# Performance work log

Hardware: AMD Instinct MI355X
Metric: run time of the kernel (lower is better)

## Reference

```python
import jax, jax.numpy as jnp
import numpy as np

BN_EPS = 1e-5


def setup_inputs() -> dict:
    key = jax.random.key(0)
    ks = jax.random.split(key, 6)
    N, E, D = 100000, 1600000, 128
    feat = jax.random.normal(ks[0], (N, D), dtype=jnp.float32)
    src = jax.random.randint(ks[1], (E,), 0, N, dtype=jnp.int32)
    dst = jax.random.randint(ks[2], (E,), 0, N, dtype=jnp.int32)
    edge_weight = jax.random.uniform(ks[3], (E,), dtype=jnp.float32)
    # GraphConv linear weight/bias (glorot-ish init)
    W = jax.random.normal(ks[4], (D, D), dtype=jnp.float32) * (1.0 / np.sqrt(D))
    b = jnp.zeros((D,), dtype=jnp.float32)
    # PReLU slopes (nn.PReLU() default single param = 0.25)
    a1 = jnp.full((1,), 0.25, dtype=jnp.float32)
    a2 = jnp.full((1,), 0.25, dtype=jnp.float32)
    # BatchNorm affine params
    gamma = jnp.ones((D,), dtype=jnp.float32)
    beta = jnp.zeros((D,), dtype=jnp.float32)
    return {"feat": feat, "src": src, "dst": dst, "edge_weight": edge_weight,
            "W": W, "b": b, "a1": a1, "gamma": gamma, "beta": beta, "a2": a2}


def _prelu(x, a):
    return jnp.where(x >= 0, x, a * x)


def reference(feat, src, dst, edge_weight, W, b, a1, gamma, beta, a2):
    N = feat.shape[0]
    # Dropout is identity at inference.
    # GraphConv norm='none': edge-weighted neighbor sum (gather-scale-scatter)
    msg = feat[src] * edge_weight[:, None]              # [E, D]
    agg = jax.ops.segment_sum(msg, dst, num_segments=N)  # [N, D]
    h = agg @ W + b                                      # [N, D]
    h = _prelu(h, a1)                                    # conv activation
    # BatchNorm over nodes (training-mode batch stats, biased var)
    mean = h.mean(axis=0)
    var = h.var(axis=0)
    h = (h - mean) / jnp.sqrt(var + BN_EPS) * gamma + beta
    h = _prelu(h, a2)                                    # outer PReLU
    return h
```

## Files before the change

### kernel.cpp

```cpp
#include <hip/hip_runtime.h>

#define D 128
#define BN_EPS 1e-5f
#define CHUNKA 8192
#define NBCAP 512
#define MAXSEGH 3072

typedef __attribute__((ext_vector_type(8))) short bf16x8;
typedef __attribute__((ext_vector_type(8))) unsigned short u16x8;
typedef __attribute__((ext_vector_type(4))) float f32x4;

__device__ __forceinline__ unsigned short f2bf(float f) {
    unsigned int u = __float_as_uint(f);
    u += 0x7FFFu + ((u >> 16) & 1u);
    return (unsigned short)(u >> 16);
}
__device__ __forceinline__ float bf2f(unsigned short u) {
    return __uint_as_float(((unsigned int)u) << 16);
}

__global__ __launch_bounds__(256) void hist_prep_kernel(
    const int* __restrict__ dst, int* __restrict__ bhist,
    const float* __restrict__ W, unsigned short* __restrict__ wswz,
    int E, int NB)
{
    __shared__ int lcnt[NBCAP];
    int t = threadIdx.x;
    if (blockIdx.x < 64) {
        int i = blockIdx.x * 256 + t;
        int j  = i & 7;
        int l  = (i >> 3) & 63;
        int c  = (i >> 9) & 7;
        int ks = i >> 12;
        int k   = ks * 32 + ((l >> 4) * 8) + j;
        int col = c * 16 + (l & 15);
        wswz[i] = f2bf(W[k * D + col]);
        return;
    }
    for (int k = t; k < NB; k += 256) lcnt[k] = 0;
    __syncthreads();
    int i = (blockIdx.x - 64) * 256 + t;
    int stride = (gridDim.x - 64) * 256;
    for (; i < E; i += stride) atomicAdd(&lcnt[dst[i] >> 8], 1);
    __syncthreads();
    for (int k = t; k < NB; k += 256) {
        int c = lcnt[k];
        if (c) atomicAdd(&bhist[k], c);
    }
}

__global__ __launch_bounds__(1024) void bucket_scan_kernel(
    const int* __restrict__ bhist, int* __restrict__ bseg,
    int* __restrict__ bcur, int NB, int E)
{
    __shared__ int part[1024];
    int t = threadIdx.x;
    int v = (t < NB) ? bhist[t] : 0;
    part[t] = v;
    __syncthreads();
    for (int d = 1; d < 1024; d <<= 1) {
        int val = (t >= d) ? part[t - d] : 0;
        __syncthreads();
        part[t] += val;
        __syncthreads();
    }
    if (t < NB) {
        int run = part[t] - v;
        bseg[t] = run;
        bcur[t] = run;
    }
    if (t == 1023) bseg[NB] = E;
}

__global__ __launch_bounds__(1024) void partition_feat_kernel(
    const int* __restrict__ src, const int* __restrict__ dst,
    const float* __restrict__ ew, int* __restrict__ bcur,
    int2* __restrict__ csr,
    const float* __restrict__ feat, unsigned short* __restrict__ featb,
    long n8, int E, int NB)
{
    __shared__ int lcnt[NBCAP];
    __shared__ int lcur[NBCAP];
    int t = threadIdx.x;
    int bid = blockIdx.x;
    int nchunks = gridDim.x / 3;
    int rem = bid % 3;
    if (rem != 0) {
        long fb = (long)(bid / 3) * 2 + (rem - 1);
        long i = fb * 1024 + t;
        long stride = (long)(2 * nchunks) * 1024;
        for (; i < n8; i += stride) {
            float4 a = *reinterpret_cast<const float4*>(feat + i * 8);
            float4 b = *reinterpret_cast<const float4*>(feat + i * 8 + 4);
            u16x8 o;
            o[0] = f2bf(a.x); o[1] = f2bf(a.y); o[2] = f2bf(a.z); o[3] = f2bf(a.w);
            o[4] = f2bf(b.x); o[5] = f2bf(b.y); o[6] = f2bf(b.z); o[7] = f2bf(b.w);
            reinterpret_cast<u16x8*>(featb)[i] = o;
        }
        return;
    }
    int base = (bid / 3) * CHUNKA;
    int lim = min(CHUNKA, E - base);
    for (int k = t; k < NB; k += 1024) lcnt[k] = 0;
    __syncthreads();
    for (int j = t; j < lim; j += 1024)
        atomicAdd(&lcnt[dst[base + j] >> 8], 1);
    __syncthreads();
    for (int k = t; k < NB; k += 1024) {
        int cnt = lcnt[k];
        lcur[k] = cnt > 0 ? atomicAdd(&bcur[k], cnt) : 0;
    }
    __syncthreads();
    for (int j = t; j < lim; j += 1024) {
        int e = base + j;
        int dv = dst[e];
        int p = atomicAdd(&lcur[dv >> 8], 1);
        csr[p] = make_int2((src[e] & 0xFFFFF) | ((dv & 255) << 20),
                           __float_as_int(ew[e]));
    }
}

__global__ __launch_bounds__(512) void bucket_sort_agg_kernel(
    const unsigned short* __restrict__ featb, const int2* __restrict__ csr,
    const int* __restrict__ bseg, unsigned short* __restrict__ aggb, int N)
{
    __shared__ int   lsrc[MAXSEGH];
    __shared__ float lwf[MAXSEGH];
    __shared__ int cnt[128];
    __shared__ int nstart[128];
    __shared__ int ncur[128];
    int t = threadIdx.x;
    int k = blockIdx.x >> 1;
    int h = blockIdx.x & 1;
    int segbeg = bseg[k], segend = bseg[k + 1];
    long nlo = ((long)k << 8) + (h << 7);
    if (t < 128) cnt[t] = 0;
    __syncthreads();
    for (int j = segbeg + t; j < segend; j += 512) {
        int s = (csr[j].x >> 20) & 255;
        if ((s >> 7) == h) atomicAdd(&cnt[s & 127], 1);
    }
    __syncthreads();
    int v = (t < 128) ? cnt[t] : 0;
    if (t < 128) nstart[t] = v;
    __syncthreads();
    for (int d = 1; d < 128; d <<= 1) {
        int val = (t >= d && t < 128) ? nstart[t - d] : 0;
        __syncthreads();
        if (t < 128) nstart[t] += val;
        __syncthreads();
    }
    int total = nstart[127];
    __syncthreads();
    if (t < 128) { int e = nstart[t] - v; nstart[t] = e; ncur[t] = e; }
    __syncthreads();

    int g = t >> 4;
    int q = (t & 15) << 3;

    if (total <= MAXSEGH) {
        for (int j = segbeg + t; j < segend; j += 512) {
            int2 e = csr[j];
            int s = (e.x >> 20) & 255;
            if ((s >> 7) == h) {
                int p = atomicAdd(&ncur[s & 127], 1);
                lsrc[p] = e.x & 0xFFFFF;
                lwf[p]  = __int_as_float(e.y);
            }
        }
        __syncthreads();
        #pragma unroll
        for (int r = 0; r < 4; ++r) {
            int n = r * 32 + g;
            int beg = nstart[n];
            int end = ncur[n];
            float acc0[8] = {0.f,0.f,0.f,0.f,0.f,0.f,0.f,0.f};
            float acc1[8] = {0.f,0.f,0.f,0.f,0.f,0.f,0.f,0.f};
            int i = beg;
            for (; i + 2 <= end; i += 2) {
                int s0 = lsrc[i], s1 = lsrc[i + 1];
                float w0 = lwf[i], w1 = lwf[i + 1];
                u16x8 v0 = *reinterpret_cast<const u16x8*>(featb + (long)s0 * D + q);
                u16x8 v1 = *reinterpret_cast<const u16x8*>(featb + (long)s1 * D + q);
                #pragma unroll
                for (int jj = 0; jj < 8; ++jj) {
                    acc0[jj] += bf2f(v0[jj]) * w0;
                    acc1[jj] += bf2f(v1[jj]) * w1;
                }
            }
            if (i < end) {
                int s0 = lsrc[i];
                float w0 = lwf[i];
                u16x8 v0 = *reinterpret_cast<const u16x8*>(featb + (long)s0 * D + q);
                #pragma unroll
                for (int jj = 0; jj < 8; ++jj) acc0[jj] += bf2f(v0[jj]) * w0;
            }
            long row = nlo + n;
            if (row < N) {
                u16x8 o;
                #pragma unroll
                for (int jj = 0; jj < 8; ++jj) o[jj] = f2bf(acc0[jj] + acc1[jj]);
                *reinterpret_cast<u16x8*>(aggb + row * D + q) = o;
            }
        }
    } else {
        #pragma unroll
        for (int r = 0; r < 4; ++r) {
            int n = r * 32 + g;
            int target = (h << 7) | n;
            float acc[8] = {0.f,0.f,0.f,0.f,0.f,0.f,0.f,0.f};
            for (int j = segbeg; j < segend; ++j) {
                int2 e = csr[j];
                if (((e.x >> 20) & 255) == target) {
                    float w = __int_as_float(e.y);
                    u16x8 vv = *reinterpret_cast<const u16x8*>(
                        featb + (long)(e.x & 0xFFFFF) * D + q);
                    #pragma unroll
                    for (int jj = 0; jj < 8; ++jj) acc[jj] += bf2f(vv[jj]) * w;
                }
            }
            long row = nlo + n;
            if (row < N) {
                u16x8 o;
                #pragma unroll
                for (int jj = 0; jj < 8; ++jj) o[jj] = f2bf(acc[jj]);
                *reinterpret_cast<u16x8*>(aggb + row * D + q) = o;
            }
        }
    }
}

__global__ __launch_bounds__(256) void gemm_stats_mfma_kernel(
    const unsigned short* aggb, const unsigned short* __restrict__ wswz,
    const float* __restrict__ bg, const float* __restrict__ a1p,
    unsigned short* houtb, float* __restrict__ stats, int N)
{
    __shared__ unsigned short Bl[16384];
    __shared__ float sblk[2][D];

    int t = threadIdx.x;
    for (int i = t; i < 2048; i += 256)
        reinterpret_cast<float4*>(Bl)[i] = reinterpret_cast<const float4*>(wswz)[i];
    if (t < D) { sblk[0][t] = 0.f; sblk[1][t] = 0.f; }
    __syncthreads();

    const int lane = t & 63;
    const int wv   = t >> 6;
    const long rbase = (long)blockIdx.x * 128 + wv * 32;
    const int lr = lane & 15;
    const int lk = lane >> 4;

    f32x4 acc[2][8];
    #pragma unroll
    for (int rt = 0; rt < 2; ++rt)
        #pragma unroll
        for (int c = 0; c < 8; ++c)
            acc[rt][c] = (f32x4){0.f, 0.f, 0.f, 0.f};

    long r0 = rbase + lr;
    long r1 = rbase + 16 + lr;
    long r0c = (r0 < N) ? r0 : 0;
    long r1c = (r1 < N) ? r1 : 0;

    #pragma unroll
    for (int ks = 0; ks < 4; ++ks) {
        bf16x8 a0 = *reinterpret_cast<const bf16x8*>(aggb + r0c * D + ks * 32 + lk * 8);
        bf16x8 a1f = *reinterpret_cast<const bf16x8*>(aggb + r1c * D + ks * 32 + lk * 8);
        #pragma unroll
        for (int c = 0; c < 8; ++c) {
            bf16x8 bfr = *reinterpret_cast<const bf16x8*>(&Bl[((ks * 8 + c) * 64 + lane) * 8]);
            acc[0][c] = __builtin_amdgcn_mfma_f32_16x16x32_bf16(a0, bfr, acc[0][c], 0, 0, 0);
            acc[1][c] = __builtin_amdgcn_mfma_f32_16x16x32_bf16(a1f, bfr, acc[1][c], 0, 0, 0);
        }
    }

    const float a1v = a1p[0];
    float bias[8];
    #pragma unroll
    for (int c = 0; c < 8; ++c) bias[c] = bg[c * 16 + lr];

    float csum[8] = {0,0,0,0,0,0,0,0};
    float csq[8]  = {0,0,0,0,0,0,0,0};
    #pragma unroll
    for (int rt = 0; rt < 2; ++rt) {
        #pragma unroll
        for (int reg = 0; reg < 4; ++reg) {
            long row = rbase + rt * 16 + lk * 4 + reg;
            if (row >= N) continue;
            #pragma unroll
            for (int c = 0; c < 8; ++c) {
                float v = acc[rt][c][reg] + bias[c];
                v = v >= 0.f ? v : v * a1v;
                houtb[row * D + c * 16 + lr] = f2bf(v);
                csum[c] += v;
                csq[c]  += v * v;
            }
        }
    }
    #pragma unroll
    for (int c = 0; c < 8; ++c) {
        atomicAdd(&sblk[0][c * 16 + lr], csum[c]);
        atomicAdd(&sblk[1][c * 16 + lr], csq[c]);
    }
    __syncthreads();
    if (t < D) {
        atomicAdd(&stats[t],     sblk[0][t]);
        atomicAdd(&stats[D + t], sblk[1][t]);
    }
}

__global__ void finalize_kernel(const float* __restrict__ stats,
                                const float* __restrict__ gamma,
                                const float* __restrict__ beta,
                                float* __restrict__ ss, int N)
{
    int c = threadIdx.x;
    float invN = 1.0f / (float)N;
    float mean = stats[c] * invN;
    float var  = stats[D + c] * invN - mean * mean;
    float sc = gamma[c] * rsqrtf(var + BN_EPS);
    ss[c]     = sc;
    ss[D + c] = beta[c] - mean * sc;
}

__global__ __launch_bounds__(256) void bn_prelu_bf16_kernel(
    const unsigned short* __restrict__ hb, const float* __restrict__ ss,
    const float* __restrict__ a2, float* __restrict__ out, long n8)
{
    const float a2v = a2[0];
    long i = (long)blockIdx.x * blockDim.x + threadIdx.x;
    long stride = (long)gridDim.x * blockDim.x;
    for (; i < n8; i += stride) {
        u16x8 hv = reinterpret_cast<const u16x8*>(hb)[i];
        int c0 = ((int)i & 15) << 3;
        float4 sc0 = *reinterpret_cast<const float4*>(ss + c0);
        float4 sc1 = *reinterpret_cast<const float4*>(ss + c0 + 4);
        float4 sh0 = *reinterpret_cast<const float4*>(ss + D + c0);
        float4 sh1 = *reinterpret_cast<const float4*>(ss + D + c0 + 4);
        float4 o0, o1;
        float v;
        v = bf2f(hv[0]) * sc0.x + sh0.x; o0.x = v >= 0.f ? v : v * a2v;
        v = bf2f(hv[1]) * sc0.y + sh0.y; o0.y = v >= 0.f ? v : v * a2v;
        v = bf2f(hv[2]) * sc0.z + sh0.z; o0.z = v >= 0.f ? v : v * a2v;
        v = bf2f(hv[3]) * sc0.w + sh0.w; o0.w = v >= 0.f ? v : v * a2v;
        v = bf2f(hv[4]) * sc1.x + sh1.x; o1.x = v >= 0.f ? v : v * a2v;
        v = bf2f(hv[5]) * sc1.y + sh1.y; o1.y = v >= 0.f ? v : v * a2v;
        v = bf2f(hv[6]) * sc1.z + sh1.z; o1.z = v >= 0.f ? v : v * a2v;
        v = bf2f(hv[7]) * sc1.w + sh1.w; o1.w = v >= 0.f ? v : v * a2v;
        *reinterpret_cast<float4*>(out + i * 8)     = o0;
        *reinterpret_cast<float4*>(out + i * 8 + 4) = o1;
    }
}

__global__ __launch_bounds__(256) void scatter_kernel(
    const float* __restrict__ feat, const int* __restrict__ src,
    const int* __restrict__ dst, const float* __restrict__ ew,
    float* __restrict__ agg, int E)
{
    long tid = (long)blockIdx.x * blockDim.x + threadIdx.x;
    int e = (int)(tid >> 5);
    if (e >= E) return;
    int q = ((int)tid & 31) << 2;
    int s = src[e];
    int d = dst[e];
    float w = ew[e];
    float4 v = *reinterpret_cast<const float4*>(feat + (long)s * D + q);
    float* o = agg + (long)d * D + q;
    atomicAdd(o + 0, v.x * w);
    atomicAdd(o + 1, v.y * w);
    atomicAdd(o + 2, v.z * w);
    atomicAdd(o + 3, v.w * w);
}

__global__ __launch_bounds__(256) void gemm_stats_kernel(
    const float* __restrict__ agg, const float* __restrict__ Wg,
    const float* __restrict__ bg, const float* __restrict__ a1,
    float* __restrict__ hout, float* __restrict__ stats, int N)
{
    __shared__ float Wl[D * D];
    __shared__ float sblk[2][D];

    int t = threadIdx.x;
    for (int i = t; i < D * D / 4; i += 256) {
        reinterpret_cast<float4*>(Wl)[i] =
            reinterpret_cast<const float4*>(Wg)[i];
    }
    if (t < D) { sblk[0][t] = 0.f; sblk[1][t] = 0.f; }
    __syncthreads();

    const int c0 = (t & 31) << 2;
    const int rbase = blockIdx.x * 32 + (t >> 5) * 4;
    const float a1v = a1[0];

    bool valid[4];
    #pragma unroll
    for (int i = 0; i < 4; ++i) valid[i] = (rbase + i) < N;

    float acc[4][4];
    float4 bv = *reinterpret_cast<const float4*>(bg + c0);
    #pragma unroll
    for (int i = 0; i < 4; ++i) {
        acc[i][0] = bv.x; acc[i][1] = bv.y; acc[i][2] = bv.z; acc[i][3] = bv.w;
    }

    for (int k0 = 0; k0 < D; k0 += 4) {
        float4 a[4];
        #pragma unroll
        for (int i = 0; i < 4; ++i) {
            a[i] = valid[i]
                ? *reinterpret_cast<const float4*>(agg + (long)(rbase + i) * D + k0)
                : make_float4(0.f, 0.f, 0.f, 0.f);
        }
        #pragma unroll
        for (int kk = 0; kk < 4; ++kk) {
            float4 wv = *reinterpret_cast<const float4*>(&Wl[(k0 + kk) * D + c0]);
            #pragma unroll
            for (int i = 0; i < 4; ++i) {
                float av = kk == 0 ? a[i].x : kk == 1 ? a[i].y : kk == 2 ? a[i].z : a[i].w;
                acc[i][0] += av * wv.x;
                acc[i][1] += av * wv.y;
                acc[i][2] += av * wv.z;
                acc[i][3] += av * wv.w;
            }
        }
    }

    float csum[4] = {0.f, 0.f, 0.f, 0.f};
    float csq[4]  = {0.f, 0.f, 0.f, 0.f};
    #pragma unroll
    for (int i = 0; i < 4; ++i) {
        if (!valid[i]) continue;
        float4 o;
        #pragma unroll
        for (int j = 0; j < 4; ++j) {
            float v = acc[i][j];
            v = v >= 0.f ? v : v * a1v;
            (&o.x)[j] = v;
            csum[j] += v;
            csq[j]  += v * v;
        }
        *reinterpret_cast<float4*>(hout + (long)(rbase + i) * D + c0) = o;
    }
    #pragma unroll
    for (int j = 0; j < 4; ++j) {
        atomicAdd(&sblk[0][c0 + j], csum[j]);
        atomicAdd(&sblk[1][c0 + j], csq[j]);
    }
    __syncthreads();
    if (t < D) {
        atomicAdd(&stats[t],     sblk[0][t]);
        atomicAdd(&stats[D + t], sblk[1][t]);
    }
}

__global__ __launch_bounds__(256) void bn_prelu_kernel(
    float* __restrict__ h, const float* __restrict__ ss,
    const float* __restrict__ a2, long n4)
{
    const float a2v = a2[0];
    long i = (long)blockIdx.x * blockDim.x + threadIdx.x;
    long stride = (long)gridDim.x * blockDim.x;
    for (; i < n4; i += stride) {
        float4 x = reinterpret_cast<float4*>(h)[i];
        int c0 = ((int)(i & 31)) << 2;
        float4 sc = *reinterpret_cast<const float4*>(ss + c0);
        float4 sh = *reinterpret_cast<const float4*>(ss + D + c0);
        float v;
        v = x.x * sc.x + sh.x; x.x = v >= 0.f ? v : v * a2v;
        v = x.y * sc.y + sh.y; x.y = v >= 0.f ? v : v * a2v;
        v = x.z * sc.z + sh.z; x.z = v >= 0.f ? v : v * a2v;
        v = x.w * sc.w + sh.w; x.w = v >= 0.f ? v : v * a2v;
        reinterpret_cast<float4*>(h)[i] = x;
    }
}

extern "C" void kernel_launch(void* const* d_in, const int* in_sizes, int n_in,
                              void* d_out, int out_size, void* d_ws, size_t ws_size,
                              hipStream_t stream)
{
    const float* feat  = (const float*)d_in[0];
    const int*   src   = (const int*)d_in[1];
    const int*   dst   = (const int*)d_in[2];
    const float* ew    = (const float*)d_in[3];
    const float* W     = (const float*)d_in[4];
    const float* b     = (const float*)d_in[5];
    const float* a1    = (const float*)d_in[6];
    const float* gamma = (const float*)d_in[7];
    const float* beta  = (const float*)d_in[8];
    const float* a2    = (const float*)d_in[9];

    const int N = in_sizes[0] / D;
    const int E = in_sizes[1];

    char* p = (char*)d_ws;
    unsigned short* featb = (unsigned short*)p; p += (size_t)N * D * sizeof(unsigned short);
    unsigned short* aggb  = (unsigned short*)p; p += (size_t)N * D * sizeof(unsigned short);
    int2* csr = (int2*)p;                 p += (size_t)E * sizeof(int2);
    int*   bseg  = (int*)p;               p += (NBCAP + 4) * sizeof(int);
    int*   bcur  = (int*)p;               p += NBCAP * sizeof(int);
    int*   bhist = (int*)p;               p += NBCAP * sizeof(int);
    float* stats = (float*)p;             p += 2 * D * sizeof(float);
    unsigned short* wswz = (unsigned short*)p; p += 16384 * sizeof(unsigned short);
    float* ss    = (float*)p;             p += 2 * D * sizeof(float);
    size_t need = (size_t)(p - (char*)d_ws);
    float* out = (float*)d_out;

    int NB = (N + 255) / 256;

    if (ws_size >= need && NB <= NBCAP) {
        hipMemsetAsync(bhist, 0, NBCAP * sizeof(int) + 2 * D * sizeof(float), stream);
        hist_prep_kernel<<<64 + 512, 256, 0, stream>>>(dst, bhist, W, wswz, E, NB);
        bucket_scan_kernel<<<1, 1024, 0, stream>>>(bhist, bseg, bcur, NB, E);
        long n8 = (long)N * D / 8;
        int nchunks = (E + CHUNKA - 1) / CHUNKA;
        partition_feat_kernel<<<3 * nchunks, 1024, 0, stream>>>(
            src, dst, ew, bcur, csr, feat, featb, n8, E, NB);
        bucket_sort_agg_kernel<<<2 * NB, 512, 0, stream>>>(featb, csr, bseg, aggb, N);
        int gblocks = (N + 127) / 128;
        gemm_stats_mfma_kernel<<<gblocks, 256, 0, stream>>>(aggb, wswz, b, a1, aggb, stats, N);
        finalize_kernel<<<1, D, 0, stream>>>(stats, gamma, beta, ss, N);
        bn_prelu_bf16_kernel<<<2048, 256, 0, stream>>>(aggb, ss, a2, out, n8);
    } else {
        float* agg = (float*)d_ws;
        stats = agg + (size_t)N * D;
        ss    = stats + 2 * D;
        hipMemsetAsync(agg, 0, ((size_t)N * D + 2 * D) * sizeof(float), stream);
        long nthreads = (long)E * 32;
        int sblocks = (int)((nthreads + 255) / 256);
        scatter_kernel<<<sblocks, 256, 0, stream>>>(feat, src, dst, ew, agg, E);
        int gblocks = (N + 31) / 32;
        gemm_stats_kernel<<<gblocks, 256, 0, stream>>>(agg, W, b, a1, out, stats, N);
        finalize_kernel<<<1, D, 0, stream>>>(stats, gamma, beta, ss, N);
        long n4 = (long)N * D / 4;
        bn_prelu_kernel<<<2048, 256, 0, stream>>>(out, ss, a2, n4);
    }
}
```

Measured before the change: 199.5 us.

## Stage partitioned edges in LDS for coalesced CSR writes, unroll gather by four

The partition kernel now loads each edge once into registers and computes a local exclusive scan of bucket counts. It scatters edges into a shared-memory staging buffer grouped by bucket, then writes them to the global CSR array in contiguous runs. Before, each edge was scattered straight to global memory and dst was read twice. The aggregation loop also moves from two to four edges per iteration, keeping more feature loads in flight. The cost is heavy LDS use (about 80KB per block, which may limit occupancy) and extra barriers in the scan.

```diff
diff --git a/kernel.cpp b/kernel.cpp
--- a/kernel.cpp
+++ b/kernel.cpp
@@ -79,8 +79,12 @@
     const float* __restrict__ feat, unsigned short* __restrict__ featb,
     long n8, int E, int NB)
 {
+    __shared__ int2 sedge[CHUNKA];
+    __shared__ unsigned short sbkt[CHUNKA];
     __shared__ int lcnt[NBCAP];
+    __shared__ int lstart[NBCAP];
     __shared__ int lcur[NBCAP];
+    __shared__ int gbase[NBCAP];
     int t = threadIdx.x;
     int bid = blockIdx.x;
     int nchunks = gridDim.x / 3;
@@ -103,20 +107,52 @@
     int lim = min(CHUNKA, E - base);
     for (int k = t; k < NB; k += 1024) lcnt[k] = 0;
     __syncthreads();
-    for (int j = t; j < lim; j += 1024)
-        atomicAdd(&lcnt[dst[base + j] >> 8], 1);
-    __syncthreads();
-    for (int k = t; k < NB; k += 1024) {
-        int cnt = lcnt[k];
-        lcur[k] = cnt > 0 ? atomicAdd(&bcur[k], cnt) : 0;
-    }
-    __syncthreads();
-    for (int j = t; j < lim; j += 1024) {
-        int e = base + j;
-        int dv = dst[e];
-        int p = atomicAdd(&lcur[dv >> 8], 1);
-        csr[p] = make_int2((src[e] & 0xFFFFF) | ((dv & 255) << 20),
-                           __float_as_int(ew[e]));
+    int dv[8]; int sv[8]; float wv[8];
+    #pragma unroll
+    for (int j = 0; j < 8; ++j) {
+        int idx = base + j * 1024 + t;
+        bool ok = (j * 1024 + t) < lim;
+        dv[j] = ok ? dst[idx] : -1;
+        sv[j] = ok ? src[idx] : 0;
+        wv[j] = ok ? ew[idx] : 0.f;
+        if (ok) atomicAdd(&lcnt[dv[j] >> 8], 1);
+    }
+    __syncthreads();
+    {
+        int v = (t < NB) ? lcnt[t] : 0;
+        if (t < 512) lstart[t < NB ? t : (NB - 1)] = 0;
+        __syncthreads();
+        if (t < 512) lstart[t] = (t < NB) ? v : 0;
+        __syncthreads();
+        for (int d = 1; d < 512; d <<= 1) {
+            int val = (t < 512 && t >= d) ? lstart[t - d] : 0;
+            __syncthreads();
+            if (t < 512) lstart[t] += val;
+            __syncthreads();
+        }
+        if (t < NB) {
+            int excl = lstart[t] - v;
+            lcur[t] = excl;
+            gbase[t] = (v > 0) ? atomicAdd(&bcur[t], v) : 0;
+        }
+        __syncthreads();
+        if (t < NB) lstart[t] = lcur[t];
+        __syncthreads();
+    }
+    #pragma unroll
+    for (int j = 0; j < 8; ++j) {
+        if (dv[j] >= 0) {
+            int b = dv[j] >> 8;
+            int p = atomicAdd(&lcur[b], 1);
+            sedge[p] = make_int2((sv[j] & 0xFFFFF) | ((dv[j] & 255) << 20),
+                                 __float_as_int(wv[j]));
+            sbkt[p] = (unsigned short)b;
+        }
+    }
+    __syncthreads();
+    for (int p = t; p < lim; p += 1024) {
+        int b = sbkt[p];
+        csr[gbase[b] + (p - lstart[b])] = sedge[p];
     }
 }
 
@@ -177,18 +213,27 @@
             float acc0[8] = {0.f,0.f,0.f,0.f,0.f,0.f,0.f,0.f};
             float acc1[8] = {0.f,0.f,0.f,0.f,0.f,0.f,0.f,0.f};
             int i = beg;
-            for (; i + 2 <= end; i += 2) {
-                int s0 = lsrc[i], s1 = lsrc[i + 1];
-                float w0 = lwf[i], w1 = lwf[i + 1];
+            for (; i + 4 <= end; i += 4) {
+                int s0 = lsrc[i],     s1 = lsrc[i + 1];
+                int s2 = lsrc[i + 2], s3 = lsrc[i + 3];
+                float w0 = lwf[i],     w1 = lwf[i + 1];
+                float w2 = lwf[i + 2], w3 = lwf[i + 3];
                 u16x8 v0 = *reinterpret_cast<const u16x8*>(featb + (long)s0 * D + q);
                 u16x8 v1 = *reinterpret_cast<const u16x8*>(featb + (long)s1 * D + q);
+                u16x8 v2 = *reinterpret_cast<const u16x8*>(featb + (long)s2 * D + q);
+                u16x8 v3 = *reinterpret_cast<const u16x8*>(featb + (long)s3 * D + q);
                 #pragma unroll
                 for (int jj = 0; jj < 8; ++jj) {
                     acc0[jj] += bf2f(v0[jj]) * w0;
                     acc1[jj] += bf2f(v1[jj]) * w1;
                 }
-            }
-            if (i < end) {
+                #pragma unroll
+                for (int jj = 0; jj < 8; ++jj) {
+                    acc0[jj] += bf2f(v2[jj]) * w2;
+                    acc1[jj] += bf2f(v3[jj]) * w3;
+                }
+            }
+            for (; i < end; ++i) {
                 int s0 = lsrc[i];
                 float w0 = lwf[i];
                 u16x8 v0 = *reinterpret_cast<const u16x8*>(featb + (long)s0 * D + q);
```

Result: no change. 197.2 us (-1.2%).
